# Optimization experiments

Hardware: AMD Instinct MI355X
Metric: run time of the kernel (lower is better)

Reference implementation:

```python
import jax, jax.numpy as jnp
import numpy as np

N_NODES = 50000
N_EDGES = 400000
HEADS = 3
CH = 128
NEG_SLOPE = 0.2
EPS = 1e-16


def setup_inputs() -> dict:
    key = jax.random.key(0)
    ks = jax.random.split(key, 10)
    return {
        "x": jax.random.normal(ks[0], (N_NODES, 9), jnp.float32),
        "emb_w": jax.random.normal(ks[1], (9, 128), jnp.float32) * 0.1,
        "emb_b": jax.random.normal(ks[2], (128,), jnp.float32) * 0.1,
        "gat_w": jax.random.normal(ks[3], (128, HEADS * CH), jnp.float32) * 0.05,
        "att_src": jax.random.normal(ks[4], (HEADS, CH), jnp.float32) * 0.1,
        "att_dst": jax.random.normal(ks[5], (HEADS, CH), jnp.float32) * 0.1,
        "gat_bias": jax.random.normal(ks[6], (CH,), jnp.float32) * 0.1,
        "out_w": jax.random.normal(ks[7], (128, 4), jnp.float32) * 0.1,
        "out_b": jax.random.normal(ks[8], (4,), jnp.float32) * 0.1,
        "edge_index": jax.random.randint(ks[9], (2, N_EDGES), 0, N_NODES, jnp.int64 if jax.config.jax_enable_x64 else jnp.int32),
    }


def reference(x, emb_w, emb_b, gat_w, att_src, att_dst, gat_bias, out_w, out_b, edge_index):
    n = x.shape[0]
    h = x @ emb_w + emb_b                                   # [N,128]
    # add self loops (PyG GATConv default)
    loops = jnp.arange(n, dtype=edge_index.dtype)
    src = jnp.concatenate([edge_index[0], loops])
    dst = jnp.concatenate([edge_index[1], loops])
    xh = (h @ gat_w).reshape(n, HEADS, CH)                  # [N,H,C]
    a_src = jnp.einsum('nhc,hc->nh', xh, att_src)           # [N,H]
    a_dst = jnp.einsum('nhc,hc->nh', xh, att_dst)           # [N,H]
    e = a_src[src] + a_dst[dst]                             # [E,H]
    e = jax.nn.leaky_relu(e, NEG_SLOPE)
    # segment softmax over destination node
    e_max = jax.ops.segment_max(e, dst, num_segments=n)
    e = jnp.exp(e - e_max[dst])
    denom = jax.ops.segment_sum(e, dst, num_segments=n)
    alpha = e / (denom[dst] + EPS)                          # [E,H]
    msg = xh[src] * alpha[:, :, None]                       # [E,H,C]
    agg = jax.ops.segment_sum(msg, dst, num_segments=n)     # [N,H,C]
    out = agg.mean(axis=1) + gat_bias                       # concat=False -> head mean
    x_new = out + h                                         # residual
    return x_new @ out_w + out_b                            # [N,4]
```

## Files before the change

kernel.cpp:

```cpp
#include <hip/hip_runtime.h>
#include <hip/hip_bf16.h>
#include <cstdint>

#define NEG 0.2f
#define SBS 256
#define PADK 56

typedef __attribute__((ext_vector_type(8))) short bf16x8;
typedef __attribute__((ext_vector_type(8))) unsigned short ushort8;
typedef __attribute__((ext_vector_type(4))) float f32x4;

__device__ __forceinline__ float bf2f(unsigned short u){
  return __uint_as_float(((unsigned)u)<<16);
}
__device__ __forceinline__ unsigned short f2bf(float f){
  __hip_bfloat16 b = __float2bfloat16(f);
  return *reinterpret_cast<unsigned short*>(&b);
}

__global__ __launch_bounds__(256)
void embed_kernel(const float* __restrict__ x, const float* __restrict__ emb_w,
                  const float* __restrict__ emb_b, const float* __restrict__ gat_w,
                  const float* __restrict__ att_src, const float* __restrict__ att_dst,
                  unsigned short* __restrict__ h_bf, float* __restrict__ a_s,
                  float* __restrict__ a_d, int* __restrict__ deg, int nN)
{
  __shared__ float watt[768];
  int tid = threadIdx.x;

  #pragma unroll
  for (int r=0;r<3;r++){
    int o = tid + r*256;
    int isD = (o >= 384);
    int t2 = isD ? (o-384) : o;
    int h = t2 >> 7, k = t2 & 127;
    const float* att = isD ? (att_dst + h*128) : (att_src + h*128);
    const float* gw  = gat_w + (size_t)k*384 + h*128;
    float dot = 0.f;
    #pragma unroll 8
    for (int c=0;c<128;c++) dot += gw[c]*att[c];
    watt[o] = dot;
  }
  __syncthreads();

  int n = blockIdx.x*256 + tid;
  if (n < nN) deg[n] = 0;
  if (n >= nN) return;

  float xv[9];
  #pragma unroll
  for (int k=0;k<9;k++) xv[k] = x[(size_t)n*9 + k];

  float s0=0.f,s1=0.f,s2=0.f, d0=0.f,d1=0.f,d2=0.f;
  unsigned short* hrow = h_bf + (size_t)n*128;

  #pragma unroll 4
  for (int c0=0; c0<128; c0+=8){
    unsigned short pk[8];
    #pragma unroll
    for (int j=0;j<8;j++){
      int c = c0 + j;
      float acc = emb_b[c];
      #pragma unroll
      for (int k=0;k<9;k++) acc += xv[k]*emb_w[k*128+c];
      pk[j] = f2bf(acc);
      s0 += acc*watt[c]; s1 += acc*watt[128+c]; s2 += acc*watt[256+c];
      d0 += acc*watt[384+c]; d1 += acc*watt[512+c]; d2 += acc*watt[640+c];
    }
    *(int4*)(hrow + c0) = *(int4*)pk;
  }
  a_s[(size_t)n*3+0]=s0; a_s[(size_t)n*3+1]=s1; a_s[(size_t)n*3+2]=s2;
  a_d[(size_t)n*3+0]=d0; a_d[(size_t)n*3+1]=d1; a_d[(size_t)n*3+2]=d2;
}

__global__ __launch_bounds__(256)
void deg_kernel(const int* __restrict__ ei, int* __restrict__ deg,
                const float* __restrict__ gat_w,
                unsigned short* __restrict__ Bt2, int nE, int ebN)
{
  if (blockIdx.x < (unsigned)ebN){
    int e = blockIdx.x*256 + threadIdx.x;
    if (e < nE){
      atomicAdd(&deg[ei[nE + e]], 1);
    }
  } else {
    int i = (blockIdx.x - ebN)*256 + threadIdx.x;
    if (i < 12*128*32){
      int ks  = i >> 12;
      int rem = i & 4095;
      int col = rem >> 5;
      int kk  = rem & 31;
      int t = ks*32 + kk;
      int h = t >> 7, k = t & 127;
      Bt2[i] = f2bf(gat_w[(size_t)k*384 + h*128 + col] * (1.f/3.f));
    }
  }
}

__global__ __launch_bounds__(SBS)
void blocksum_kernel(const int* __restrict__ deg, int* __restrict__ bsum, int nN)
{
  int i = blockIdx.x*SBS + threadIdx.x;
  int v = (i < nN) ? deg[i] : 0;
  #pragma unroll
  for (int off=32; off; off>>=1) v += __shfl_down(v, off);
  __shared__ int ws[SBS/64];
  if ((threadIdx.x&63)==0) ws[threadIdx.x>>6] = v;
  __syncthreads();
  if (threadIdx.x==0){
    int s=0;
    #pragma unroll
    for (int i2=0;i2<SBS/64;i2++) s += ws[i2];
    bsum[blockIdx.x]=s;
  }
}

__global__ __launch_bounds__(256)
void scansum_kernel(const int* __restrict__ bsum, int* __restrict__ boff, int nB)
{
  __shared__ int s[256];
  int t = threadIdx.x;
  int v = (t < nB) ? bsum[t] : 0;
  s[t] = v;
  __syncthreads();
  for (int off=1; off<256; off<<=1){
    int add = (t >= off) ? s[t-off] : 0;
    __syncthreads();
    s[t] += add;
    __syncthreads();
  }
  if (t < nB) boff[t] = (t==0) ? 0 : s[t-1];
}

__global__ __launch_bounds__(SBS)
void blockscan_kernel(const int* __restrict__ deg, const int* __restrict__ boff,
                      int* __restrict__ rowptr, int* __restrict__ cursor, int nN)
{
  __shared__ int s[SBS];
  int t = threadIdx.x;
  int i = blockIdx.x*SBS + t;
  int v = (i < nN) ? deg[i] : 0;
  s[t] = v;
  __syncthreads();
  for (int off=1; off<SBS; off<<=1){
    int add = (t >= off) ? s[t-off] : 0;
    __syncthreads();
    s[t] += add;
    __syncthreads();
  }
  int excl = boff[blockIdx.x] + ((t==0) ? 0 : s[t-1]);
  if (i < nN){ rowptr[i] = excl; cursor[i] = excl; }
  if (i == nN-1) rowptr[nN] = excl + v;
}

__global__ __launch_bounds__(256)
void scatter_kernel(const int* __restrict__ ei, int* __restrict__ cursor,
                    int* __restrict__ csr, int nE)
{
  int e = blockIdx.x*256 + threadIdx.x;
  if (e < nE){
    int s = ei[e], d = ei[nE + e];
    int pos = atomicAdd(&cursor[d], 1);
    csr[pos] = s;
  }
}

__global__ __launch_bounds__(256)
void gather_kernel(const int* __restrict__ rowptr, const int* __restrict__ csr,
                   const float* __restrict__ a_s, const float* __restrict__ a_d,
                   const unsigned short* __restrict__ h_bf,
                   unsigned short* __restrict__ hagg, int nN)
{
  int wave = threadIdx.x >> 6, lane = threadIdx.x & 63;
  int g   = lane >> 3;
  int lin = lane & 7;
  int gb  = lane & 56;
  int n = blockIdx.x*32 + wave*8 + g;
  int valid = (n < nN);
  int nc = valid ? n : (nN-1);

  int ro  = rowptr[nc];
  int deg = rowptr[nc+1] - ro;
  int degT = valid ? (deg + 1) : 0;

  float ad0 = a_d[(size_t)nc*3+0], ad1 = a_d[(size_t)nc*3+1], ad2 = a_d[(size_t)nc*3+2];

  float a0[16], a1[16], a2[16];
  #pragma unroll
  for (int c=0;c<16;c++){ a0[c]=0.f; a1[c]=0.f; a2[c]=0.f; }
  float d0=0.f, d1=0.f, d2=0.f;

  const unsigned short* hb = h_bf + 16*lin;

  for (int base=0; base<degT; base+=8){
    int i = base + lin;
    int sReg = nc; float p0=0.f, p1=0.f, p2=0.f;
    if (i < degT){
      int s = (i < deg) ? csr[ro+i] : nc;
      sReg = s;
      float e0 = a_s[(size_t)s*3+0] + ad0; e0 = e0>0.f ? e0 : NEG*e0;
      float e1 = a_s[(size_t)s*3+1] + ad1; e1 = e1>0.f ? e1 : NEG*e1;
      float e2 = a_s[(size_t)s*3+2] + ad2; e2 = e2>0.f ? e2 : NEG*e2;
      p0 = __expf(e0); p1 = __expf(e1); p2 = __expf(e2);
      d0 += p0; d1 += p1; d2 += p2;
    }
    int cnt = min(8, degT - base);
    int j = 0;
    for (; j+1 < cnt; j += 2){
      int   sA = __shfl(sReg, gb+j);
      int   sB = __shfl(sReg, gb+j+1);
      float A0 = __shfl(p0, gb+j),   A1 = __shfl(p1, gb+j),   A2 = __shfl(p2, gb+j);
      float B0 = __shfl(p0, gb+j+1), B1 = __shfl(p1, gb+j+1), B2 = __shfl(p2, gb+j+1);
      const unsigned short* ra = hb + (size_t)sA*128;
      const unsigned short* rb = hb + (size_t)sB*128;
      ushort8 ha0 = *(const ushort8*)(ra), ha1 = *(const ushort8*)(ra+8);
      ushort8 hb0 = *(const ushort8*)(rb), hb1 = *(const ushort8*)(rb+8);
      #pragma unroll
      for (int c=0;c<8;c++){
        float fa = bf2f(ha0[c]), fb = bf2f(hb0[c]);
        a0[c] += A0*fa + B0*fb;
        a1[c] += A1*fa + B1*fb;
        a2[c] += A2*fa + B2*fb;
      }
      #pragma unroll
      for (int c=0;c<8;c++){
        float fa = bf2f(ha1[c]), fb = bf2f(hb1[c]);
        a0[8+c] += A0*fa + B0*fb;
        a1[8+c] += A1*fa + B1*fb;
        a2[8+c] += A2*fa + B2*fb;
      }
    }
    if (j < cnt){
      int   sA = __shfl(sReg, gb+j);
      float A0 = __shfl(p0, gb+j), A1 = __shfl(p1, gb+j), A2 = __shfl(p2, gb+j);
      const unsigned short* ra = hb + (size_t)sA*128;
      ushort8 ha0 = *(const ushort8*)(ra), ha1 = *(const ushort8*)(ra+8);
      #pragma unroll
      for (int c=0;c<8;c++){
        float fa = bf2f(ha0[c]);
        a0[c] += A0*fa; a1[c] += A1*fa; a2[c] += A2*fa;
      }
      #pragma unroll
      for (int c=0;c<8;c++){
        float fa = bf2f(ha1[c]);
        a0[8+c] += A0*fa; a1[8+c] += A1*fa; a2[8+c] += A2*fa;
      }
    }
  }

  #pragma unroll
  for (int off=1; off<8; off<<=1){
    d0 += __shfl_xor(d0, off);
    d1 += __shfl_xor(d1, off);
    d2 += __shfl_xor(d2, off);
  }

  if (valid){
    float w0 = 1.f/(d0+1e-16f);
    float w1 = 1.f/(d1+1e-16f);
    float w2 = 1.f/(d2+1e-16f);
    unsigned short o0[16], o1[16], o2[16];
    #pragma unroll
    for (int c=0;c<16;c++){
      o0[c] = f2bf(a0[c]*w0);
      o1[c] = f2bf(a1[c]*w1);
      o2[c] = f2bf(a2[c]*w2);
    }
    size_t bi = (size_t)n*384 + 16*lin;
    *(int4*)(hagg + bi      ) = *(int4*)(o0);
    *(int4*)(hagg + bi +   8) = *(int4*)(o0+8);
    *(int4*)(hagg + bi + 128) = *(int4*)(o1);
    *(int4*)(hagg + bi + 136) = *(int4*)(o1+8);
    *(int4*)(hagg + bi + 256) = *(int4*)(o2);
    *(int4*)(hagg + bi + 264) = *(int4*)(o2+8);
  }
}

__global__ __launch_bounds__(256)
void gemm2_kernel(const unsigned short* __restrict__ hagg,
                  const unsigned short* __restrict__ Bt2,
                  const unsigned short* __restrict__ h_bf,
                  const float* __restrict__ gat_bias,
                  const float* __restrict__ out_w, const float* __restrict__ out_b,
                  float* __restrict__ out, int nN)
{
  __shared__ __align__(16) unsigned short Bs[2][128*PADK];
  int tid  = threadIdx.x;
  int wave = tid >> 6, lane = tid & 63;
  int cl = lane & 15, kg = lane >> 4;
  int r0 = blockIdx.x*64 + wave*16;
  int rowA = min(r0 + cl, nN-1);
  const unsigned short* aBase = hagg + (size_t)rowA*384 + kg*8;

  int scol = tid >> 1, shalf = tid & 1;
  int dstI = scol*(PADK/8) + shalf*2;

  {
    const int4* src = (const int4*)Bt2;
    int4 t0 = src[2*tid], t1 = src[2*tid+1];
    ((int4*)Bs[0])[dstI]   = t0;
    ((int4*)Bs[0])[dstI+1] = t1;
  }
  f32x4 acc[8];
  #pragma unroll
  for (int f=0;f<8;f++) acc[f] = (f32x4){0.f,0.f,0.f,0.f};
  bf16x8 aCur = *(const bf16x8*)(aBase);
  __syncthreads();

  #pragma unroll
  for (int ks=0; ks<12; ks++){
    int4 t0, t1; bf16x8 aNext;
    if (ks < 11){
      const int4* src = (const int4*)(Bt2 + (size_t)(ks+1)*4096);
      t0 = src[2*tid]; t1 = src[2*tid+1];
      aNext = *(const bf16x8*)(aBase + (ks+1)*32);
    }
    const unsigned short* bs = Bs[ks & 1];
    #pragma unroll
    for (int f=0;f<8;f++){
      bf16x8 b = *(const bf16x8*)(bs + (f*16 + cl)*PADK + kg*8);
      acc[f] = __builtin_amdgcn_mfma_f32_16x16x32_bf16(aCur, b, acc[f], 0, 0, 0);
    }
    if (ks < 11){
      int4* dst = (int4*)Bs[(ks+1) & 1];
      dst[dstI]   = t0;
      dst[dstI+1] = t1;
      aCur = aNext;
    }
    __syncthreads();
  }

  float p[4][4];
  #pragma unroll
  for (int r=0;r<4;r++)
    #pragma unroll
    for (int j=0;j<4;j++) p[r][j]=0.f;

  #pragma unroll
  for (int f=0;f<8;f++){
    int col = f*16 + cl;
    float bias = gat_bias[col];
    float w0=out_w[col*4+0], w1=out_w[col*4+1], w2=out_w[col*4+2], w3=out_w[col*4+3];
    #pragma unroll
    for (int r=0;r<4;r++){
      int row = r0 + kg*4 + r;
      float hres = (row < nN) ? bf2f(h_bf[(size_t)row*128 + col]) : 0.f;
      float xn = acc[f][r] + bias + hres;
      p[r][0] += xn*w0; p[r][1] += xn*w1; p[r][2] += xn*w2; p[r][3] += xn*w3;
    }
  }
  #pragma unroll
  for (int off=1; off<16; off<<=1){
    #pragma unroll
    for (int r=0;r<4;r++)
      #pragma unroll
      for (int j=0;j<4;j++) p[r][j] += __shfl_xor(p[r][j], off);
  }
  if (cl == 0){
    #pragma unroll
    for (int r=0;r<4;r++){
      int row = r0 + kg*4 + r;
      if (row < nN){
        float4 o = {p[r][0]+out_b[0], p[r][1]+out_b[1], p[r][2]+out_b[2], p[r][3]+out_b[3]};
        *(float4*)(out + (size_t)row*4) = o;
      }
    }
  }
}

extern "C" void kernel_launch(void* const* d_in, const int* in_sizes, int n_in,
                              void* d_out, int out_size, void* d_ws, size_t ws_size,
                              hipStream_t stream) {
  const float* x       = (const float*)d_in[0];
  const float* emb_w   = (const float*)d_in[1];
  const float* emb_b   = (const float*)d_in[2];
  const float* gat_w   = (const float*)d_in[3];
  const float* att_src = (const float*)d_in[4];
  const float* att_dst = (const float*)d_in[5];
  const float* gat_bias= (const float*)d_in[6];
  const float* out_w   = (const float*)d_in[7];
  const float* out_b   = (const float*)d_in[8];
  const int*   ei      = (const int*)d_in[9];
  float* out = (float*)d_out;

  int nN = in_sizes[0]/9;
  int nE = in_sizes[9]/2;
  int nB = (nN + SBS - 1) / SBS;
  int ebN = (nE + 255)/256;

  char* p = (char*)d_ws;
  auto alloc = [&](size_t bytes)->char*{
    char* r = p; p += (bytes + 255) & ~(size_t)255; return r;
  };
  unsigned short* h_bf   = (unsigned short*)alloc((size_t)nN*128*2);
  float*          a_s    = (float*)         alloc((size_t)nN*3*4);
  float*          a_d    = (float*)         alloc((size_t)nN*3*4);
  unsigned short* Bt2    = (unsigned short*)alloc((size_t)12*128*32*2);
  int*            deg    = (int*)           alloc((size_t)nN*4);
  int*            rowptr = (int*)           alloc(((size_t)nN+1)*4);
  int*            cursor = (int*)           alloc((size_t)nN*4);
  int*            csr    = (int*)           alloc((size_t)nE*4);
  int*            bsum   = (int*)           alloc((size_t)nB*4);
  int*            boff   = (int*)           alloc((size_t)nB*4);
  unsigned short* hagg   = (unsigned short*)alloc((size_t)nN*384*2);

  embed_kernel<<<nB, 256, 0, stream>>>(
      x, emb_w, emb_b, gat_w, att_src, att_dst, h_bf, a_s, a_d, deg, nN);

  deg_kernel<<<ebN + 192, 256, 0, stream>>>(ei, deg, gat_w, Bt2, nE, ebN);

  blocksum_kernel<<<nB, SBS, 0, stream>>>(deg, bsum, nN);
  scansum_kernel<<<1, 256, 0, stream>>>(bsum, boff, nB);
  blockscan_kernel<<<nB, SBS, 0, stream>>>(deg, boff, rowptr, cursor, nN);
  scatter_kernel<<<ebN, 256, 0, stream>>>(ei, cursor, csr, nE);

  gather_kernel<<<(nN+31)/32, 256, 0, stream>>>(
      rowptr, csr, a_s, a_d, h_bf, hagg, nN);

  gemm2_kernel<<<(nN+63)/64, 256, 0, stream>>>(
      hagg, Bt2, h_bf, gat_bias, out_w, out_b, out, nN);
}
```

Baseline: 211.8 us.

## Fuse CSR construction kernels into one cooperative kernel with grid syncs

```diff
diff --git a/kernel.cpp b/kernel.cpp
--- a/kernel.cpp
+++ b/kernel.cpp
@@ -1,10 +1,14 @@
 #include <hip/hip_runtime.h>
 #include <hip/hip_bf16.h>
+#include <hip/hip_cooperative_groups.h>
 #include <cstdint>
+
+namespace cg = cooperative_groups;
 
 #define NEG 0.2f
 #define SBS 256
 #define PADK 56
+#define COOP_BLOCKS 1024
 
 typedef __attribute__((ext_vector_type(8))) short bf16x8;
 typedef __attribute__((ext_vector_type(8))) unsigned short ushort8;
@@ -23,11 +27,25 @@
                   const float* __restrict__ emb_b, const float* __restrict__ gat_w,
                   const float* __restrict__ att_src, const float* __restrict__ att_dst,
                   unsigned short* __restrict__ h_bf, float* __restrict__ a_s,
-                  float* __restrict__ a_d, int* __restrict__ deg, int nN)
+                  float* __restrict__ a_d, unsigned short* __restrict__ Bt2,
+                  int nN, int nB)
 {
+  int tid = threadIdx.x;
+  if ((int)blockIdx.x >= nB){
+    int i = (blockIdx.x - nB)*256 + tid;
+    if (i < 12*128*32){
+      int ks  = i >> 12;
+      int rem = i & 4095;
+      int col = rem >> 5;
+      int kk  = rem & 31;
+      int t = ks*32 + kk;
+      int h = t >> 7, k = t & 127;
+      Bt2[i] = f2bf(gat_w[(size_t)k*384 + h*128 + col] * (1.f/3.f));
+    }
+    return;
+  }
+
   __shared__ float watt[768];
-  int tid = threadIdx.x;
-
   #pragma unroll
   for (int r=0;r<3;r++){
     int o = tid + r*256;
@@ -44,7 +62,6 @@
   __syncthreads();
 
   int n = blockIdx.x*256 + tid;
-  if (n < nN) deg[n] = 0;
   if (n >= nN) return;
 
   float xv[9];
@@ -74,91 +91,73 @@
 }
 
 __global__ __launch_bounds__(256)
-void deg_kernel(const int* __restrict__ ei, int* __restrict__ deg,
-                const float* __restrict__ gat_w,
-                unsigned short* __restrict__ Bt2, int nE, int ebN)
+void csr_coop(const int* __restrict__ ei, int* __restrict__ deg,
+              int* __restrict__ bsum, int* __restrict__ boff,
+              int* __restrict__ rowptr, int* __restrict__ cursor,
+              int* __restrict__ csr, int nN, int nE, int nB)
 {
-  if (blockIdx.x < (unsigned)ebN){
-    int e = blockIdx.x*256 + threadIdx.x;
-    if (e < nE){
-      atomicAdd(&deg[ei[nE + e]], 1);
-    }
-  } else {
-    int i = (blockIdx.x - ebN)*256 + threadIdx.x;
-    if (i < 12*128*32){
-      int ks  = i >> 12;
-      int rem = i & 4095;
-      int col = rem >> 5;
-      int kk  = rem & 31;
-      int t = ks*32 + kk;
-      int h = t >> 7, k = t & 127;
-      Bt2[i] = f2bf(gat_w[(size_t)k*384 + h*128 + col] * (1.f/3.f));
-    }
-  }
-}
-
-__global__ __launch_bounds__(SBS)
-void blocksum_kernel(const int* __restrict__ deg, int* __restrict__ bsum, int nN)
-{
-  int i = blockIdx.x*SBS + threadIdx.x;
-  int v = (i < nN) ? deg[i] : 0;
-  #pragma unroll
-  for (int off=32; off; off>>=1) v += __shfl_down(v, off);
-  __shared__ int ws[SBS/64];
-  if ((threadIdx.x&63)==0) ws[threadIdx.x>>6] = v;
-  __syncthreads();
-  if (threadIdx.x==0){
-    int s=0;
-    #pragma unroll
-    for (int i2=0;i2<SBS/64;i2++) s += ws[i2];
-    bsum[blockIdx.x]=s;
-  }
-}
-
-__global__ __launch_bounds__(256)
-void scansum_kernel(const int* __restrict__ bsum, int* __restrict__ boff, int nB)
-{
-  __shared__ int s[256];
-  int t = threadIdx.x;
-  int v = (t < nB) ? bsum[t] : 0;
-  s[t] = v;
-  __syncthreads();
-  for (int off=1; off<256; off<<=1){
-    int add = (t >= off) ? s[t-off] : 0;
+  cg::grid_group grid = cg::this_grid();
+  int tid  = threadIdx.x;
+  int gtid = blockIdx.x*256 + tid;
+  int gsz  = gridDim.x*256;
+
+  for (int i=gtid; i<nN; i+=gsz) deg[i] = 0;
+  grid.sync();
+
+  for (int e=gtid; e<nE; e+=gsz) atomicAdd(&deg[ei[nE + e]], 1);
+  grid.sync();
+
+  if ((int)blockIdx.x < nB){
+    int i = blockIdx.x*SBS + tid;
+    int v = (i < nN) ? deg[i] : 0;
+    #pragma unroll
+    for (int off=32; off; off>>=1) v += __shfl_down(v, off);
+    __shared__ int ws[SBS/64];
+    if ((tid&63)==0) ws[tid>>6] = v;
     __syncthreads();
-    s[t] += add;
+    if (tid==0){
+      int s=0;
+      #pragma unroll
+      for (int i2=0;i2<SBS/64;i2++) s += ws[i2];
+      bsum[blockIdx.x]=s;
+    }
+  }
+  grid.sync();
+
+  if (blockIdx.x == 0){
+    __shared__ int s[256];
+    int v = (tid < nB) ? bsum[tid] : 0;
+    s[tid] = v;
     __syncthreads();
-  }
-  if (t < nB) boff[t] = (t==0) ? 0 : s[t-1];
-}
-
-__global__ __launch_bounds__(SBS)
-void blockscan_kernel(const int* __restrict__ deg, const int* __restrict__ boff,
-                      int* __restrict__ rowptr, int* __restrict__ cursor, int nN)
-{
-  __shared__ int s[SBS];
-  int t = threadIdx.x;
-  int i = blockIdx.x*SBS + t;
-  int v = (i < nN) ? deg[i] : 0;
-  s[t] = v;
-  __syncthreads();
-  for (int off=1; off<SBS; off<<=1){
-    int add = (t >= off) ? s[t-off] : 0;
+    for (int off=1; off<256; off<<=1){
+      int add = (tid >= off) ? s[tid-off] : 0;
+      __syncthreads();
+      s[tid] += add;
+      __syncthreads();
+    }
+    if (tid < nB) boff[tid] = (tid==0) ? 0 : s[tid-1];
+  }
+  grid.sync();
+
+  if ((int)blockIdx.x < nB){
+    __shared__ int s[SBS];
+    int i = blockIdx.x*SBS + tid;
+    int v = (i < nN) ? deg[i] : 0;
+    s[tid] = v;
     __syncthreads();
-    s[t] += add;
-    __syncthreads();
-  }
-  int excl = boff[blockIdx.x] + ((t==0) ? 0 : s[t-1]);
-  if (i < nN){ rowptr[i] = excl; cursor[i] = excl; }
-  if (i == nN-1) rowptr[nN] = excl + v;
-}
-
-__global__ __launch_bounds__(256)
-void scatter_kernel(const int* __restrict__ ei, int* __restrict__ cursor,
-                    int* __restrict__ csr, int nE)
-{
-  int e = blockIdx.x*256 + threadIdx.x;
-  if (e < nE){
+    for (int off=1; off<SBS; off<<=1){
+      int add = (tid >= off) ? s[tid-off] : 0;
+      __syncthreads();
+      s[tid] += add;
+      __syncthreads();
+    }
+    int excl = boff[blockIdx.x] + ((tid==0) ? 0 : s[tid-1]);
+    if (i < nN){ rowptr[i] = excl; cursor[i] = excl; }
+    if (i == nN-1) rowptr[nN] = excl + v;
+  }
+  grid.sync();
+
+  for (int e=gtid; e<nE; e+=gsz){
     int s = ei[e], d = ei[nE + e];
     int pos = atomicAdd(&cursor[d], 1);
     csr[pos] = s;
@@ -386,7 +385,6 @@
   int nN = in_sizes[0]/9;
   int nE = in_sizes[9]/2;
   int nB = (nN + SBS - 1) / SBS;
-  int ebN = (nE + 255)/256;
 
   char* p = (char*)d_ws;
   auto alloc = [&](size_t bytes)->char*{
@@ -404,15 +402,24 @@
   int*            boff   = (int*)           alloc((size_t)nB*4);
   unsigned short* hagg   = (unsigned short*)alloc((size_t)nN*384*2);
 
-  embed_kernel<<<nB, 256, 0, stream>>>(
-      x, emb_w, emb_b, gat_w, att_src, att_dst, h_bf, a_s, a_d, deg, nN);
-
-  deg_kernel<<<ebN + 192, 256, 0, stream>>>(ei, deg, gat_w, Bt2, nE, ebN);
-
-  blocksum_kernel<<<nB, SBS, 0, stream>>>(deg, bsum, nN);
-  scansum_kernel<<<1, 256, 0, stream>>>(bsum, boff, nB);
-  blockscan_kernel<<<nB, SBS, 0, stream>>>(deg, boff, rowptr, cursor, nN);
-  scatter_kernel<<<ebN, 256, 0, stream>>>(ei, cursor, csr, nE);
+  embed_kernel<<<nB + 192, 256, 0, stream>>>(
+      x, emb_w, emb_b, gat_w, att_src, att_dst, h_bf, a_s, a_d, Bt2, nN, nB);
+
+  {
+    const int* ei_   = ei;
+    int* deg_    = deg;
+    int* bsum_   = bsum;
+    int* boff_   = boff;
+    int* rowptr_ = rowptr;
+    int* cursor_ = cursor;
+    int* csr_    = csr;
+    int nN_ = nN, nE_ = nE, nB_ = nB;
+    void* args[] = { (void*)&ei_, (void*)&deg_, (void*)&bsum_, (void*)&boff_,
+                     (void*)&rowptr_, (void*)&cursor_, (void*)&csr_,
+                     (void*)&nN_, (void*)&nE_, (void*)&nB_ };
+    hipLaunchCooperativeKernel((const void*)csr_coop, dim3(COOP_BLOCKS), dim3(256),
+                               args, 0, stream);
+  }
 
   gather_kernel<<<(nN+31)/32, 256, 0, stream>>>(
       rowptr, csr, a_s, a_d, h_bf, hagg, nN);
```

New measurement: 680.9 us. +221.5%, slower.

## Precompute edge attention weights in scatter and store packed float4 CSR values

Applied to the files above, without the earlier changes.

```diff
diff --git a/kernel.cpp b/kernel.cpp
--- a/kernel.cpp
+++ b/kernel.cpp
@@ -80,9 +80,7 @@
 {
   if (blockIdx.x < (unsigned)ebN){
     int e = blockIdx.x*256 + threadIdx.x;
-    if (e < nE){
-      atomicAdd(&deg[ei[nE + e]], 1);
-    }
+    if (e < nE) atomicAdd(&deg[ei[nE + e]], 1);
   } else {
     int i = (blockIdx.x - ebN)*256 + threadIdx.x;
     if (i < 12*128*32){
@@ -101,7 +99,7 @@
 void blocksum_kernel(const int* __restrict__ deg, int* __restrict__ bsum, int nN)
 {
   int i = blockIdx.x*SBS + threadIdx.x;
-  int v = (i < nN) ? deg[i] : 0;
+  int v = (i < nN) ? deg[i]+1 : 0;
   #pragma unroll
   for (int off=32; off; off>>=1) v += __shfl_down(v, off);
   __shared__ int ws[SBS/64];
@@ -139,7 +137,7 @@
   __shared__ int s[SBS];
   int t = threadIdx.x;
   int i = blockIdx.x*SBS + t;
-  int v = (i < nN) ? deg[i] : 0;
+  int v = (i < nN) ? deg[i]+1 : 0;
   s[t] = v;
   __syncthreads();
   for (int off=1; off<SBS; off<<=1){
@@ -155,124 +153,99 @@
 
 __global__ __launch_bounds__(256)
 void scatter_kernel(const int* __restrict__ ei, int* __restrict__ cursor,
-                    int* __restrict__ csr, int nE)
-{
-  int e = blockIdx.x*256 + threadIdx.x;
-  if (e < nE){
-    int s = ei[e], d = ei[nE + e];
-    int pos = atomicAdd(&cursor[d], 1);
-    csr[pos] = s;
-  }
-}
-
-__global__ __launch_bounds__(256)
-void gather_kernel(const int* __restrict__ rowptr, const int* __restrict__ csr,
-                   const float* __restrict__ a_s, const float* __restrict__ a_d,
+                    const float* __restrict__ a_s, const float* __restrict__ a_d,
+                    const int* __restrict__ rowptr, float4* __restrict__ val,
+                    int nE, int ebN, int nN)
+{
+  if (blockIdx.x < (unsigned)ebN){
+    int e = blockIdx.x*256 + threadIdx.x;
+    if (e < nE){
+      int s = ei[e], d = ei[nE + e];
+      float e0 = a_s[(size_t)s*3+0] + a_d[(size_t)d*3+0]; e0 = e0>0.f ? e0 : NEG*e0;
+      float e1 = a_s[(size_t)s*3+1] + a_d[(size_t)d*3+1]; e1 = e1>0.f ? e1 : NEG*e1;
+      float e2 = a_s[(size_t)s*3+2] + a_d[(size_t)d*3+2]; e2 = e2>0.f ? e2 : NEG*e2;
+      int pos = atomicAdd(&cursor[d], 1);
+      val[pos] = make_float4(__expf(e0), __expf(e1), __expf(e2), __int_as_float(s));
+    }
+  } else {
+    int n = (blockIdx.x - ebN)*256 + threadIdx.x;
+    if (n < nN){
+      float e0 = a_s[(size_t)n*3+0] + a_d[(size_t)n*3+0]; e0 = e0>0.f ? e0 : NEG*e0;
+      float e1 = a_s[(size_t)n*3+1] + a_d[(size_t)n*3+1]; e1 = e1>0.f ? e1 : NEG*e1;
+      float e2 = a_s[(size_t)n*3+2] + a_d[(size_t)n*3+2]; e2 = e2>0.f ? e2 : NEG*e2;
+      val[rowptr[n+1]-1] = make_float4(__expf(e0), __expf(e1), __expf(e2),
+                                       __int_as_float(n));
+    }
+  }
+}
+
+__global__ __launch_bounds__(256)
+void gather_kernel(const int* __restrict__ rowptr, const float4* __restrict__ val,
                    const unsigned short* __restrict__ h_bf,
                    unsigned short* __restrict__ hagg, int nN)
 {
   int wave = threadIdx.x >> 6, lane = threadIdx.x & 63;
-  int g   = lane >> 3;
-  int lin = lane & 7;
-  int gb  = lane & 56;
-  int n = blockIdx.x*32 + wave*8 + g;
+  int g   = lane >> 4;
+  int lin = lane & 15;
+  int n = blockIdx.x*16 + wave*4 + g;
   int valid = (n < nN);
   int nc = valid ? n : (nN-1);
 
-  int ro  = rowptr[nc];
-  int deg = rowptr[nc+1] - ro;
-  int degT = valid ? (deg + 1) : 0;
-
-  float ad0 = a_d[(size_t)nc*3+0], ad1 = a_d[(size_t)nc*3+1], ad2 = a_d[(size_t)nc*3+2];
-
-  float a0[16], a1[16], a2[16];
-  #pragma unroll
-  for (int c=0;c<16;c++){ a0[c]=0.f; a1[c]=0.f; a2[c]=0.f; }
-  float d0=0.f, d1=0.f, d2=0.f;
-
-  const unsigned short* hb = h_bf + 16*lin;
-
-  for (int base=0; base<degT; base+=8){
-    int i = base + lin;
-    int sReg = nc; float p0=0.f, p1=0.f, p2=0.f;
-    if (i < degT){
-      int s = (i < deg) ? csr[ro+i] : nc;
-      sReg = s;
-      float e0 = a_s[(size_t)s*3+0] + ad0; e0 = e0>0.f ? e0 : NEG*e0;
-      float e1 = a_s[(size_t)s*3+1] + ad1; e1 = e1>0.f ? e1 : NEG*e1;
-      float e2 = a_s[(size_t)s*3+2] + ad2; e2 = e2>0.f ? e2 : NEG*e2;
-      p0 = __expf(e0); p1 = __expf(e1); p2 = __expf(e2);
-      d0 += p0; d1 += p1; d2 += p2;
-    }
-    int cnt = min(8, degT - base);
-    int j = 0;
-    for (; j+1 < cnt; j += 2){
-      int   sA = __shfl(sReg, gb+j);
-      int   sB = __shfl(sReg, gb+j+1);
-      float A0 = __shfl(p0, gb+j),   A1 = __shfl(p1, gb+j),   A2 = __shfl(p2, gb+j);
-      float B0 = __shfl(p0, gb+j+1), B1 = __shfl(p1, gb+j+1), B2 = __shfl(p2, gb+j+1);
-      const unsigned short* ra = hb + (size_t)sA*128;
-      const unsigned short* rb = hb + (size_t)sB*128;
-      ushort8 ha0 = *(const ushort8*)(ra), ha1 = *(const ushort8*)(ra+8);
-      ushort8 hb0 = *(const ushort8*)(rb), hb1 = *(const ushort8*)(rb+8);
-      #pragma unroll
-      for (int c=0;c<8;c++){
-        float fa = bf2f(ha0[c]), fb = bf2f(hb0[c]);
-        a0[c] += A0*fa + B0*fb;
-        a1[c] += A1*fa + B1*fb;
-        a2[c] += A2*fa + B2*fb;
-      }
-      #pragma unroll
-      for (int c=0;c<8;c++){
-        float fa = bf2f(ha1[c]), fb = bf2f(hb1[c]);
-        a0[8+c] += A0*fa + B0*fb;
-        a1[8+c] += A1*fa + B1*fb;
-        a2[8+c] += A2*fa + B2*fb;
-      }
-    }
-    if (j < cnt){
-      int   sA = __shfl(sReg, gb+j);
-      float A0 = __shfl(p0, gb+j), A1 = __shfl(p1, gb+j), A2 = __shfl(p2, gb+j);
-      const unsigned short* ra = hb + (size_t)sA*128;
-      ushort8 ha0 = *(const ushort8*)(ra), ha1 = *(const ushort8*)(ra+8);
-      #pragma unroll
-      for (int c=0;c<8;c++){
-        float fa = bf2f(ha0[c]);
-        a0[c] += A0*fa; a1[c] += A1*fa; a2[c] += A2*fa;
-      }
-      #pragma unroll
-      for (int c=0;c<8;c++){
-        float fa = bf2f(ha1[c]);
-        a0[8+c] += A0*fa; a1[8+c] += A1*fa; a2[8+c] += A2*fa;
-      }
-    }
-  }
-
-  #pragma unroll
-  for (int off=1; off<8; off<<=1){
-    d0 += __shfl_xor(d0, off);
-    d1 += __shfl_xor(d1, off);
-    d2 += __shfl_xor(d2, off);
+  int ro   = rowptr[nc];
+  int degT = valid ? (rowptr[nc+1] - ro) : 0;
+
+  float a0[8], a1[8], a2[8];
+  #pragma unroll
+  for (int c=0;c<8;c++){ a0[c]=0.f; a1[c]=0.f; a2[c]=0.f; }
+  float den0=0.f, den1=0.f, den2=0.f;
+
+  const unsigned short* hb = h_bf + 8*lin;
+  const float4* vrow = val + ro;
+
+  int j = 0;
+  for (; j+1 < degT; j += 2){
+    float4 vA = vrow[j];
+    float4 vB = vrow[j+1];
+    int sA = __float_as_int(vA.w);
+    int sB = __float_as_int(vB.w);
+    ushort8 ha = *(const ushort8*)(hb + (size_t)sA*128);
+    ushort8 hc = *(const ushort8*)(hb + (size_t)sB*128);
+    den0 += vA.x + vB.x; den1 += vA.y + vB.y; den2 += vA.z + vB.z;
+    #pragma unroll
+    for (int c=0;c<8;c++){
+      float fa = bf2f(ha[c]), fb = bf2f(hc[c]);
+      a0[c] += vA.x*fa + vB.x*fb;
+      a1[c] += vA.y*fa + vB.y*fb;
+      a2[c] += vA.z*fa + vB.z*fb;
+    }
+  }
+  if (j < degT){
+    float4 vA = vrow[j];
+    int sA = __float_as_int(vA.w);
+    ushort8 ha = *(const ushort8*)(hb + (size_t)sA*128);
+    den0 += vA.x; den1 += vA.y; den2 += vA.z;
+    #pragma unroll
+    for (int c=0;c<8;c++){
+      float fa = bf2f(ha[c]);
+      a0[c] += vA.x*fa; a1[c] += vA.y*fa; a2[c] += vA.z*fa;
+    }
   }
 
   if (valid){
-    float w0 = 1.f/(d0+1e-16f);
-    float w1 = 1.f/(d1+1e-16f);
-    float w2 = 1.f/(d2+1e-16f);
-    unsigned short o0[16], o1[16], o2[16];
-    #pragma unroll
-    for (int c=0;c<16;c++){
+    float w0 = 1.f/(den0+1e-16f);
+    float w1 = 1.f/(den1+1e-16f);
+    float w2 = 1.f/(den2+1e-16f);
+    unsigned short o0[8], o1[8], o2[8];
+    #pragma unroll
+    for (int c=0;c<8;c++){
       o0[c] = f2bf(a0[c]*w0);
       o1[c] = f2bf(a1[c]*w1);
       o2[c] = f2bf(a2[c]*w2);
     }
-    size_t bi = (size_t)n*384 + 16*lin;
-    *(int4*)(hagg + bi      ) = *(int4*)(o0);
-    *(int4*)(hagg + bi +   8) = *(int4*)(o0+8);
-    *(int4*)(hagg + bi + 128) = *(int4*)(o1);
-    *(int4*)(hagg + bi + 136) = *(int4*)(o1+8);
-    *(int4*)(hagg + bi + 256) = *(int4*)(o2);
-    *(int4*)(hagg + bi + 264) = *(int4*)(o2+8);
+    size_t bi = (size_t)n*384 + 8*lin;
+    *(int4*)(hagg + bi      ) = *(int4*)o0;
+    *(int4*)(hagg + bi + 128) = *(int4*)o1;
+    *(int4*)(hagg + bi + 256) = *(int4*)o2;
   }
 }
 
@@ -399,9 +372,9 @@
   int*            deg    = (int*)           alloc((size_t)nN*4);
   int*            rowptr = (int*)           alloc(((size_t)nN+1)*4);
   int*            cursor = (int*)           alloc((size_t)nN*4);
-  int*            csr    = (int*)           alloc((size_t)nE*4);
   int*            bsum   = (int*)           alloc((size_t)nB*4);
   int*            boff   = (int*)           alloc((size_t)nB*4);
+  float4*         val    = (float4*)        alloc(((size_t)nE+nN)*16);
   unsigned short* hagg   = (unsigned short*)alloc((size_t)nN*384*2);
 
   embed_kernel<<<nB, 256, 0, stream>>>(
@@ -412,10 +385,12 @@
   blocksum_kernel<<<nB, SBS, 0, stream>>>(deg, bsum, nN);
   scansum_kernel<<<1, 256, 0, stream>>>(bsum, boff, nB);
   blockscan_kernel<<<nB, SBS, 0, stream>>>(deg, boff, rowptr, cursor, nN);
-  scatter_kernel<<<ebN, 256, 0, stream>>>(ei, cursor, csr, nE);
-
-  gather_kernel<<<(nN+31)/32, 256, 0, stream>>>(
-      rowptr, csr, a_s, a_d, h_bf, hagg, nN);
+
+  scatter_kernel<<<ebN + nB, 256, 0, stream>>>(
+      ei, cursor, a_s, a_d, rowptr, val, nE, ebN, nN);
+
+  gather_kernel<<<(nN+15)/16, 256, 0, stream>>>(
+      rowptr, val, h_bf, hagg, nN);
 
   gemm2_kernel<<<(nN+63)/64, 256, 0, stream>>>(
       hagg, Bt2, h_bf, gat_bias, out_w, out_b, out, nN);
```

Result: no change. 208.0 us (-1.8%).
